# Kernel optimization log

Measured on AMD Instinct MI355X. Metric: run time of the kernel, lower is better.

Reference implementation:

```python
import jax, jax.numpy as jnp
import numpy as np

N, H, O, E, K = 131072, 128, 128, 8, 2


def setup_inputs() -> dict:
    key = jax.random.key(0)
    k1, k2, k3, k4 = jax.random.split(key, 4)
    x = jax.random.normal(k1, (N, H), dtype=jnp.float32)
    w_gate = jax.random.normal(k2, (H, E), dtype=jnp.float32) * 0.02
    w_noise = jax.random.normal(k3, (H, E), dtype=jnp.float32) * 0.02
    w_expert = jax.random.normal(k4, (E, H, O), dtype=jnp.float32) * (1.0 / np.sqrt(H))
    b_expert = jnp.zeros((E, O), dtype=jnp.float32)
    return {"x": x, "w_gate": w_gate, "w_noise": w_noise,
            "w_expert": w_expert, "b_expert": b_expert, "top_k": K}


def _gates(x, w_gate, top_k):
    # Noisy top-k gating (eval mode: noise term w_noise is inactive).
    logits = x @ w_gate                              # [N, E]
    top_vals, top_idx = jax.lax.top_k(logits, top_k)  # [N, K]
    top_gates = jax.nn.softmax(top_vals, axis=-1)     # renormalize over top-k
    n = logits.shape[0]
    rows = jnp.arange(n)[:, None]                     # [N, 1]
    gates = jnp.zeros_like(logits).at[rows, top_idx].set(top_gates)  # [N, E] sparse
    return gates


def reference(x, w_gate, w_noise, w_expert, b_expert, top_k):
    gates = _gates(x, w_gate, top_k)                                  # [N, E]
    # Dense (mathematically identical) dispatch/combine: every expert FFN
    # applied per token, weighted by its (mostly-zero) gate.
    expert_out = jnp.einsum('nh,eho->neo', x, w_expert) + b_expert     # [N, E, O]
    out = jnp.einsum('ne,neo->no', gates, expert_out)                  # [N, O]
    return out
```

## Files before the change

kernel.cpp:

```cpp
#include <hip/hip_runtime.h>
#include <math.h>

typedef __bf16 bf16x8 __attribute__((ext_vector_type(8)));
typedef float f32x16 __attribute__((ext_vector_type(16)));

#define NTOK 131072
#define HDIM 128
#define ODIM 128
#define NEXP 8

__device__ __forceinline__ unsigned short f2bf(float f){
  union { float f; unsigned u; } v; v.f = f;
  unsigned r = v.u + 0x7FFFu + ((v.u >> 16) & 1u);
  return (unsigned short)(r >> 16);
}

__global__ void pack_w(const float* __restrict__ we, const float* __restrict__ be,
                       unsigned short* __restrict__ pw){
  int f = blockIdx.x * 256 + threadIdx.x;
  int l  = f & 63;
  int kt = (f >> 6) % 9;
  int emt = f / (64 * 9);
  int mt = emt & 3;
  int e  = emt >> 2;
  int o  = (mt << 5) + (l & 31);
  unsigned short vals[8];
#pragma unroll
  for (int j = 0; j < 8; ++j){
    int kl = ((l >> 5) << 3) + j;
    float v;
    if (kt < 8){
      int h = kt * 16 + kl;
      v = we[(e * HDIM + h) * ODIM + o];
    } else {
      v = (kl == 0) ? be[e * ODIM + o] : 0.0f;
    }
    vals[j] = f2bf(v);
  }
  *(bf16x8*)(pw + (size_t)f * 8) = *(bf16x8*)vals;
}

__launch_bounds__(256, 4)
__global__ void moe_fused(const float* __restrict__ x, const float* __restrict__ wg,
                          const unsigned short* __restrict__ pw, float* __restrict__ out){
  __shared__ char lds[33792 + 4096 + 2048];
  float* xs            = (float*)lds;
  unsigned short* frag = (unsigned short*)lds;
  float* tb            = (float*)lds;
  float* wgt           = (float*)(lds + 33792);
  float* glds          = (float*)(lds + 33792 + 4096);

  int t = threadIdx.x;
  size_t tokbase = (size_t)blockIdx.x * 64;

  {
    float4 v = ((const float4*)wg)[t];
    int h = t >> 1, e0 = (t & 1) * 4;
    wgt[(e0 + 0) * 128 + h] = v.x;
    wgt[(e0 + 1) * 128 + h] = v.y;
    wgt[(e0 + 2) * 128 + h] = v.z;
    wgt[(e0 + 3) * 128 + h] = v.w;
  }
  {
    const float4* xsrc = (const float4*)(x + tokbase * HDIM);
#pragma unroll
    for (int i = 0; i < 8; ++i){
      int idx = i * 256 + t;
      int tok = idx >> 5, c = idx & 31;
      *(float4*)&xs[tok * 132 + c * 4] = xsrc[idx];
    }
  }
  __syncthreads();

  float4 cv[8];
#pragma unroll
  for (int i = 0; i < 8; ++i)
    cv[i] = *(float4*)&xs[(t >> 2) * 132 + (t & 3) * 32 + i * 4];

  {
    int tok = t & 63;
    const float* w0 = wgt + (t >> 6) * 2 * 128;
    const float* w1 = w0 + 128;
    float lg0 = 0.0f, lg1 = 0.0f;
#pragma unroll 8
    for (int c = 0; c < 32; ++c){
      float4 v = *(float4*)&xs[tok * 132 + c * 4];
      lg0 += v.x * w0[c * 4] + v.y * w0[c * 4 + 1] + v.z * w0[c * 4 + 2] + v.w * w0[c * 4 + 3];
      lg1 += v.x * w1[c * 4] + v.y * w1[c * 4 + 1] + v.z * w1[c * 4 + 2] + v.w * w1[c * 4 + 3];
    }
    int e0 = (t >> 6) * 2;
    glds[e0 * 64 + tok] = lg0;
    glds[(e0 + 1) * 64 + tok] = lg1;
  }
  __syncthreads();

  if (t < 64){
    float lg[8];
#pragma unroll
    for (int e = 0; e < 8; ++e) lg[e] = glds[e * 64 + t];
    int i1 = 0; float v1 = lg[0];
#pragma unroll
    for (int e = 1; e < 8; ++e) if (lg[e] > v1){ v1 = lg[e]; i1 = e; }
    int i2 = -1; float v2 = -3.4e38f;
#pragma unroll
    for (int e = 0; e < 8; ++e) if (e != i1 && lg[e] > v2){ v2 = lg[e]; i2 = e; }
    float ex = __expf(v2 - v1);
    float inv = 1.0f / (1.0f + ex);
#pragma unroll
    for (int e = 0; e < 8; ++e)
      glds[e * 64 + t] = (e == i1) ? inv : ((e == i2) ? ex * inv : 0.0f);
  }

  {
    int tokL = t >> 2, q = t & 3, tg = tokL >> 5;
#pragma unroll
    for (int jb = 0; jb < 4; ++jb){
      int h0 = q * 32 + jb * 8;
      int kt = h0 >> 4;
      int lslot = (tokL & 31) + 32 * ((h0 >> 3) & 1);
      float4 a = cv[2 * jb], b = cv[2 * jb + 1];
      unsigned long long lo = (unsigned long long)f2bf(a.x)
                            | ((unsigned long long)f2bf(a.y) << 16)
                            | ((unsigned long long)f2bf(a.z) << 32)
                            | ((unsigned long long)f2bf(a.w) << 48);
      unsigned long long hi = (unsigned long long)f2bf(b.x)
                            | ((unsigned long long)f2bf(b.y) << 16)
                            | ((unsigned long long)f2bf(b.z) << 32)
                            | ((unsigned long long)f2bf(b.w) << 48);
      unsigned long long* dst =
        (unsigned long long*)&frag[(((tg * 9) + kt) * 64 + lslot) * 8];
      dst[0] = lo; dst[1] = hi;
    }
    if (t < 128){
      int btg = t >> 6, bl = t & 63;
      unsigned long long* dst =
        (unsigned long long*)&frag[(((btg * 9) + 8) * 64 + bl) * 8];
      dst[0] = (bl < 32) ? 0x3F80ull : 0ull;
      dst[1] = 0ull;
    }
  }
  __syncthreads();

  int w = t >> 6, l = t & 63, l32 = l & 31, lh = l >> 5;

  f32x16 zero16;
#pragma unroll
  for (int i = 0; i < 16; ++i) zero16[i] = 0.0f;
  f32x16 tot0 = zero16, tot1 = zero16;

  const bf16x8* pwp = (const bf16x8*)pw;
#pragma unroll 1
  for (int e = 0; e < 8; ++e){
    float g0 = glds[e * 64 + l32];
    float g1 = glds[e * 64 + 32 + l32];
    const bf16x8* ap = pwp + ((size_t)(e * 4 + w) * 9) * 64 + l;
    bf16x8 a0 = ap[0 * 64], a1 = ap[1 * 64], a2 = ap[2 * 64],
           a3 = ap[3 * 64], a4 = ap[4 * 64], a5 = ap[5 * 64],
           a6 = ap[6 * 64], a7 = ap[7 * 64], a8 = ap[8 * 64];
    f32x16 p = zero16;
    p = __builtin_amdgcn_mfma_f32_32x32x16_bf16(a0, *(const bf16x8*)&frag[((0 * 9 + 0) * 64 + l) * 8], p, 0, 0, 0);
    p = __builtin_amdgcn_mfma_f32_32x32x16_bf16(a1, *(const bf16x8*)&frag[((0 * 9 + 1) * 64 + l) * 8], p, 0, 0, 0);
    p = __builtin_amdgcn_mfma_f32_32x32x16_bf16(a2, *(const bf16x8*)&frag[((0 * 9 + 2) * 64 + l) * 8], p, 0, 0, 0);
    p = __builtin_amdgcn_mfma_f32_32x32x16_bf16(a3, *(const bf16x8*)&frag[((0 * 9 + 3) * 64 + l) * 8], p, 0, 0, 0);
    p = __builtin_amdgcn_mfma_f32_32x32x16_bf16(a4, *(const bf16x8*)&frag[((0 * 9 + 4) * 64 + l) * 8], p, 0, 0, 0);
    p = __builtin_amdgcn_mfma_f32_32x32x16_bf16(a5, *(const bf16x8*)&frag[((0 * 9 + 5) * 64 + l) * 8], p, 0, 0, 0);
    p = __builtin_amdgcn_mfma_f32_32x32x16_bf16(a6, *(const bf16x8*)&frag[((0 * 9 + 6) * 64 + l) * 8], p, 0, 0, 0);
    p = __builtin_amdgcn_mfma_f32_32x32x16_bf16(a7, *(const bf16x8*)&frag[((0 * 9 + 7) * 64 + l) * 8], p, 0, 0, 0);
    p = __builtin_amdgcn_mfma_f32_32x32x16_bf16(a8, *(const bf16x8*)&frag[((0 * 9 + 8) * 64 + l) * 8], p, 0, 0, 0);
#pragma unroll
    for (int r = 0; r < 16; ++r) tot0[r] += g0 * p[r];
    __builtin_amdgcn_sched_barrier(0);
    p = zero16;
    p = __builtin_amdgcn_mfma_f32_32x32x16_bf16(a0, *(const bf16x8*)&frag[((1 * 9 + 0) * 64 + l) * 8], p, 0, 0, 0);
    p = __builtin_amdgcn_mfma_f32_32x32x16_bf16(a1, *(const bf16x8*)&frag[((1 * 9 + 1) * 64 + l) * 8], p, 0, 0, 0);
    p = __builtin_amdgcn_mfma_f32_32x32x16_bf16(a2, *(const bf16x8*)&frag[((1 * 9 + 2) * 64 + l) * 8], p, 0, 0, 0);
    p = __builtin_amdgcn_mfma_f32_32x32x16_bf16(a3, *(const bf16x8*)&frag[((1 * 9 + 3) * 64 + l) * 8], p, 0, 0, 0);
    p = __builtin_amdgcn_mfma_f32_32x32x16_bf16(a4, *(const bf16x8*)&frag[((1 * 9 + 4) * 64 + l) * 8], p, 0, 0, 0);
    p = __builtin_amdgcn_mfma_f32_32x32x16_bf16(a5, *(const bf16x8*)&frag[((1 * 9 + 5) * 64 + l) * 8], p, 0, 0, 0);
    p = __builtin_amdgcn_mfma_f32_32x32x16_bf16(a6, *(const bf16x8*)&frag[((1 * 9 + 6) * 64 + l) * 8], p, 0, 0, 0);
    p = __builtin_amdgcn_mfma_f32_32x32x16_bf16(a7, *(const bf16x8*)&frag[((1 * 9 + 7) * 64 + l) * 8], p, 0, 0, 0);
    p = __builtin_amdgcn_mfma_f32_32x32x16_bf16(a8, *(const bf16x8*)&frag[((1 * 9 + 8) * 64 + l) * 8], p, 0, 0, 0);
#pragma unroll
    for (int r = 0; r < 16; ++r) tot1[r] += g1 * p[r];
    __builtin_amdgcn_sched_barrier(0);
  }
  __syncthreads();

  {
#pragma unroll
    for (int rg = 0; rg < 4; ++rg){
      int o = w * 32 + rg * 8 + lh * 4;
      {
        int trow = 0 * 32 + l32;
        int cs = (o >> 2) ^ l32;
        *(float4*)&tb[trow * 128 + cs * 4] =
          make_float4(tot0[rg * 4 + 0], tot0[rg * 4 + 1], tot0[rg * 4 + 2], tot0[rg * 4 + 3]);
      }
      {
        int trow = 1 * 32 + l32;
        int cs = (o >> 2) ^ l32;
        *(float4*)&tb[trow * 128 + cs * 4] =
          make_float4(tot1[rg * 4 + 0], tot1[rg * 4 + 1], tot1[rg * 4 + 2], tot1[rg * 4 + 3]);
      }
    }
  }
  __syncthreads();
#pragma unroll
  for (int i = 0; i < 8; ++i){
    int idx = i * 256 + t;
    int trow = idx >> 5, c = idx & 31;
    int cs = c ^ (trow & 31);
    float4 v = *(float4*)&tb[trow * 128 + cs * 4];
    *(float4*)(out + (tokbase + trow) * ODIM + c * 4) = v;
  }
}

extern "C" void kernel_launch(void* const* d_in, const int* in_sizes, int n_in,
                              void* d_out, int out_size, void* d_ws, size_t ws_size,
                              hipStream_t stream){
  const float* x  = (const float*)d_in[0];
  const float* wg = (const float*)d_in[1];
  const float* we = (const float*)d_in[3];
  const float* be = (const float*)d_in[4];
  float* out = (float*)d_out;

  unsigned short* pw = (unsigned short*)d_ws;

  pack_w   <<<72,   256, 0, stream>>>(we, be, pw);
  moe_fused<<<2048, 256, 0, stream>>>(x, wg, pw, out);
}
```

Before: 153.3 us.

## Double block tile to 128 tokens with 512 threads per block

Each block now handles 128 tokens with 8 waves instead of 64 tokens with 4 waves. Waves are split into two token groups that share the same expert-weight column tiles. This halves the number of blocks and amortizes the per-block gate-weight load and setup over more tokens. LDS use roughly doubles to about 74KB per block, and the work is spread over fewer, larger blocks.

```diff
diff --git a/kernel.cpp b/kernel.cpp
--- a/kernel.cpp
+++ b/kernel.cpp
@@ -40,20 +40,20 @@
   *(bf16x8*)(pw + (size_t)f * 8) = *(bf16x8*)vals;
 }
 
-__launch_bounds__(256, 4)
+__launch_bounds__(512, 4)
 __global__ void moe_fused(const float* __restrict__ x, const float* __restrict__ wg,
                           const unsigned short* __restrict__ pw, float* __restrict__ out){
-  __shared__ char lds[33792 + 4096 + 2048];
+  __shared__ char lds[67584 + 4096 + 4096];
   float* xs            = (float*)lds;
   unsigned short* frag = (unsigned short*)lds;
   float* tb            = (float*)lds;
-  float* wgt           = (float*)(lds + 33792);
-  float* glds          = (float*)(lds + 33792 + 4096);
+  float* wgt           = (float*)(lds + 67584);
+  float* glds          = (float*)(lds + 67584 + 4096);
 
   int t = threadIdx.x;
-  size_t tokbase = (size_t)blockIdx.x * 64;
-
-  {
+  size_t tokbase = (size_t)blockIdx.x * 128;
+
+  if (t < 256){
     float4 v = ((const float4*)wg)[t];
     int h = t >> 1, e0 = (t & 1) * 4;
     wgt[(e0 + 0) * 128 + h] = v.x;
@@ -65,7 +65,7 @@
     const float4* xsrc = (const float4*)(x + tokbase * HDIM);
 #pragma unroll
     for (int i = 0; i < 8; ++i){
-      int idx = i * 256 + t;
+      int idx = i * 512 + t;
       int tok = idx >> 5, c = idx & 31;
       *(float4*)&xs[tok * 132 + c * 4] = xsrc[idx];
     }
@@ -78,8 +78,8 @@
     cv[i] = *(float4*)&xs[(t >> 2) * 132 + (t & 3) * 32 + i * 4];
 
   {
-    int tok = t & 63;
-    const float* w0 = wgt + (t >> 6) * 2 * 128;
+    int tok = t & 127;
+    const float* w0 = wgt + (t >> 7) * 2 * 128;
     const float* w1 = w0 + 128;
     float lg0 = 0.0f, lg1 = 0.0f;
 #pragma unroll 8
@@ -88,16 +88,16 @@
       lg0 += v.x * w0[c * 4] + v.y * w0[c * 4 + 1] + v.z * w0[c * 4 + 2] + v.w * w0[c * 4 + 3];
       lg1 += v.x * w1[c * 4] + v.y * w1[c * 4 + 1] + v.z * w1[c * 4 + 2] + v.w * w1[c * 4 + 3];
     }
-    int e0 = (t >> 6) * 2;
-    glds[e0 * 64 + tok] = lg0;
-    glds[(e0 + 1) * 64 + tok] = lg1;
-  }
-  __syncthreads();
-
-  if (t < 64){
+    int e0 = (t >> 7) * 2;
+    glds[e0 * 128 + tok] = lg0;
+    glds[(e0 + 1) * 128 + tok] = lg1;
+  }
+  __syncthreads();
+
+  if (t < 128){
     float lg[8];
 #pragma unroll
-    for (int e = 0; e < 8; ++e) lg[e] = glds[e * 64 + t];
+    for (int e = 0; e < 8; ++e) lg[e] = glds[e * 128 + t];
     int i1 = 0; float v1 = lg[0];
 #pragma unroll
     for (int e = 1; e < 8; ++e) if (lg[e] > v1){ v1 = lg[e]; i1 = e; }
@@ -108,7 +108,7 @@
     float inv = 1.0f / (1.0f + ex);
 #pragma unroll
     for (int e = 0; e < 8; ++e)
-      glds[e * 64 + t] = (e == i1) ? inv : ((e == i2) ? ex * inv : 0.0f);
+      glds[e * 128 + t] = (e == i1) ? inv : ((e == i2) ? ex * inv : 0.0f);
   }
 
   {
@@ -131,7 +131,7 @@
         (unsigned long long*)&frag[(((tg * 9) + kt) * 64 + lslot) * 8];
       dst[0] = lo; dst[1] = hi;
     }
-    if (t < 128){
+    if (t < 256){
       int btg = t >> 6, bl = t & 63;
       unsigned long long* dst =
         (unsigned long long*)&frag[(((btg * 9) + 8) * 64 + bl) * 8];
@@ -142,6 +142,7 @@
   __syncthreads();
 
   int w = t >> 6, l = t & 63, l32 = l & 31, lh = l >> 5;
+  int ot = w & 3, tgA = (w >> 2) * 2;
 
   f32x16 zero16;
 #pragma unroll
@@ -151,35 +152,35 @@
   const bf16x8* pwp = (const bf16x8*)pw;
 #pragma unroll 1
   for (int e = 0; e < 8; ++e){
-    float g0 = glds[e * 64 + l32];
-    float g1 = glds[e * 64 + 32 + l32];
-    const bf16x8* ap = pwp + ((size_t)(e * 4 + w) * 9) * 64 + l;
+    float g0 = glds[e * 128 + tgA * 32 + l32];
+    float g1 = glds[e * 128 + tgA * 32 + 32 + l32];
+    const bf16x8* ap = pwp + ((size_t)(e * 4 + ot) * 9) * 64 + l;
     bf16x8 a0 = ap[0 * 64], a1 = ap[1 * 64], a2 = ap[2 * 64],
            a3 = ap[3 * 64], a4 = ap[4 * 64], a5 = ap[5 * 64],
            a6 = ap[6 * 64], a7 = ap[7 * 64], a8 = ap[8 * 64];
     f32x16 p = zero16;
-    p = __builtin_amdgcn_mfma_f32_32x32x16_bf16(a0, *(const bf16x8*)&frag[((0 * 9 + 0) * 64 + l) * 8], p, 0, 0, 0);
-    p = __builtin_amdgcn_mfma_f32_32x32x16_bf16(a1, *(const bf16x8*)&frag[((0 * 9 + 1) * 64 + l) * 8], p, 0, 0, 0);
-    p = __builtin_amdgcn_mfma_f32_32x32x16_bf16(a2, *(const bf16x8*)&frag[((0 * 9 + 2) * 64 + l) * 8], p, 0, 0, 0);
-    p = __builtin_amdgcn_mfma_f32_32x32x16_bf16(a3, *(const bf16x8*)&frag[((0 * 9 + 3) * 64 + l) * 8], p, 0, 0, 0);
-    p = __builtin_amdgcn_mfma_f32_32x32x16_bf16(a4, *(const bf16x8*)&frag[((0 * 9 + 4) * 64 + l) * 8], p, 0, 0, 0);
-    p = __builtin_amdgcn_mfma_f32_32x32x16_bf16(a5, *(const bf16x8*)&frag[((0 * 9 + 5) * 64 + l) * 8], p, 0, 0, 0);
-    p = __builtin_amdgcn_mfma_f32_32x32x16_bf16(a6, *(const bf16x8*)&frag[((0 * 9 + 6) * 64 + l) * 8], p, 0, 0, 0);
-    p = __builtin_amdgcn_mfma_f32_32x32x16_bf16(a7, *(const bf16x8*)&frag[((0 * 9 + 7) * 64 + l) * 8], p, 0, 0, 0);
-    p = __builtin_amdgcn_mfma_f32_32x32x16_bf16(a8, *(const bf16x8*)&frag[((0 * 9 + 8) * 64 + l) * 8], p, 0, 0, 0);
+    p = __builtin_amdgcn_mfma_f32_32x32x16_bf16(a0, *(const bf16x8*)&frag[((tgA * 9 + 0) * 64 + l) * 8], p, 0, 0, 0);
+    p = __builtin_amdgcn_mfma_f32_32x32x16_bf16(a1, *(const bf16x8*)&frag[((tgA * 9 + 1) * 64 + l) * 8], p, 0, 0, 0);
+    p = __builtin_amdgcn_mfma_f32_32x32x16_bf16(a2, *(const bf16x8*)&frag[((tgA * 9 + 2) * 64 + l) * 8], p, 0, 0, 0);
+    p = __builtin_amdgcn_mfma_f32_32x32x16_bf16(a3, *(const bf16x8*)&frag[((tgA * 9 + 3) * 64 + l) * 8], p, 0, 0, 0);
+    p = __builtin_amdgcn_mfma_f32_32x32x16_bf16(a4, *(const bf16x8*)&frag[((tgA * 9 + 4) * 64 + l) * 8], p, 0, 0, 0);
+    p = __builtin_amdgcn_mfma_f32_32x32x16_bf16(a5, *(const bf16x8*)&frag[((tgA * 9 + 5) * 64 + l) * 8], p, 0, 0, 0);
+    p = __builtin_amdgcn_mfma_f32_32x32x16_bf16(a6, *(const bf16x8*)&frag[((tgA * 9 + 6) * 64 + l) * 8], p, 0, 0, 0);
+    p = __builtin_amdgcn_mfma_f32_32x32x16_bf16(a7, *(const bf16x8*)&frag[((tgA * 9 + 7) * 64 + l) * 8], p, 0, 0, 0);
+    p = __builtin_amdgcn_mfma_f32_32x32x16_bf16(a8, *(const bf16x8*)&frag[((tgA * 9 + 8) * 64 + l) * 8], p, 0, 0, 0);
 #pragma unroll
     for (int r = 0; r < 16; ++r) tot0[r] += g0 * p[r];
     __builtin_amdgcn_sched_barrier(0);
     p = zero16;
-    p = __builtin_amdgcn_mfma_f32_32x32x16_bf16(a0, *(const bf16x8*)&frag[((1 * 9 + 0) * 64 + l) * 8], p, 0, 0, 0);
-    p = __builtin_amdgcn_mfma_f32_32x32x16_bf16(a1, *(const bf16x8*)&frag[((1 * 9 + 1) * 64 + l) * 8], p, 0, 0, 0);
-    p = __builtin_amdgcn_mfma_f32_32x32x16_bf16(a2, *(const bf16x8*)&frag[((1 * 9 + 2) * 64 + l) * 8], p, 0, 0, 0);
-    p = __builtin_amdgcn_mfma_f32_32x32x16_bf16(a3, *(const bf16x8*)&frag[((1 * 9 + 3) * 64 + l) * 8], p, 0, 0, 0);
-    p = __builtin_amdgcn_mfma_f32_32x32x16_bf16(a4, *(const bf16x8*)&frag[((1 * 9 + 4) * 64 + l) * 8], p, 0, 0, 0);
-    p = __builtin_amdgcn_mfma_f32_32x32x16_bf16(a5, *(const bf16x8*)&frag[((1 * 9 + 5) * 64 + l) * 8], p, 0, 0, 0);
-    p = __builtin_amdgcn_mfma_f32_32x32x16_bf16(a6, *(const bf16x8*)&frag[((1 * 9 + 6) * 64 + l) * 8], p, 0, 0, 0);
-    p = __builtin_amdgcn_mfma_f32_32x32x16_bf16(a7, *(const bf16x8*)&frag[((1 * 9 + 7) * 64 + l) * 8], p, 0, 0, 0);
-    p = __builtin_amdgcn_mfma_f32_32x32x16_bf16(a8, *(const bf16x8*)&frag[((1 * 9 + 8) * 64 + l) * 8], p, 0, 0, 0);
+    p = __builtin_amdgcn_mfma_f32_32x32x16_bf16(a0, *(const bf16x8*)&frag[(((tgA + 1) * 9 + 0) * 64 + l) * 8], p, 0, 0, 0);
+    p = __builtin_amdgcn_mfma_f32_32x32x16_bf16(a1, *(const bf16x8*)&frag[(((tgA + 1) * 9 + 1) * 64 + l) * 8], p, 0, 0, 0);
+    p = __builtin_amdgcn_mfma_f32_32x32x16_bf16(a2, *(const bf16x8*)&frag[(((tgA + 1) * 9 + 2) * 64 + l) * 8], p, 0, 0, 0);
+    p = __builtin_amdgcn_mfma_f32_32x32x16_bf16(a3, *(const bf16x8*)&frag[(((tgA + 1) * 9 + 3) * 64 + l) * 8], p, 0, 0, 0);
+    p = __builtin_amdgcn_mfma_f32_32x32x16_bf16(a4, *(const bf16x8*)&frag[(((tgA + 1) * 9 + 4) * 64 + l) * 8], p, 0, 0, 0);
+    p = __builtin_amdgcn_mfma_f32_32x32x16_bf16(a5, *(const bf16x8*)&frag[(((tgA + 1) * 9 + 5) * 64 + l) * 8], p, 0, 0, 0);
+    p = __builtin_amdgcn_mfma_f32_32x32x16_bf16(a6, *(const bf16x8*)&frag[(((tgA + 1) * 9 + 6) * 64 + l) * 8], p, 0, 0, 0);
+    p = __builtin_amdgcn_mfma_f32_32x32x16_bf16(a7, *(const bf16x8*)&frag[(((tgA + 1) * 9 + 7) * 64 + l) * 8], p, 0, 0, 0);
+    p = __builtin_amdgcn_mfma_f32_32x32x16_bf16(a8, *(const bf16x8*)&frag[(((tgA + 1) * 9 + 8) * 64 + l) * 8], p, 0, 0, 0);
 #pragma unroll
     for (int r = 0; r < 16; ++r) tot1[r] += g1 * p[r];
     __builtin_amdgcn_sched_barrier(0);
@@ -189,15 +190,15 @@
   {
 #pragma unroll
     for (int rg = 0; rg < 4; ++rg){
-      int o = w * 32 + rg * 8 + lh * 4;
+      int o = ot * 32 + rg * 8 + lh * 4;
       {
-        int trow = 0 * 32 + l32;
+        int trow = tgA * 32 + l32;
         int cs = (o >> 2) ^ l32;
         *(float4*)&tb[trow * 128 + cs * 4] =
           make_float4(tot0[rg * 4 + 0], tot0[rg * 4 + 1], tot0[rg * 4 + 2], tot0[rg * 4 + 3]);
       }
       {
-        int trow = 1 * 32 + l32;
+        int trow = (tgA + 1) * 32 + l32;
         int cs = (o >> 2) ^ l32;
         *(float4*)&tb[trow * 128 + cs * 4] =
           make_float4(tot1[rg * 4 + 0], tot1[rg * 4 + 1], tot1[rg * 4 + 2], tot1[rg * 4 + 3]);
@@ -207,7 +208,7 @@
   __syncthreads();
 #pragma unroll
   for (int i = 0; i < 8; ++i){
-    int idx = i * 256 + t;
+    int idx = i * 512 + t;
     int trow = idx >> 5, c = idx & 31;
     int cs = c ^ (trow & 31);
     float4 v = *(float4*)&tb[trow * 128 + cs * 4];
@@ -227,5 +228,5 @@
   unsigned short* pw = (unsigned short*)d_ws;
 
   pack_w   <<<72,   256, 0, stream>>>(we, be, pw);
-  moe_fused<<<2048, 256, 0, stream>>>(x, wg, pw, out);
-}
+  moe_fused<<<1024, 512, 0, stream>>>(x, wg, pw, out);
+}
```

After: 159.4 us. 4.0% more time.
